# Optimization experiments

Measured on AMD Instinct MI355X. Metric: run time of the kernel, lower is better.

The kernel has to match this reference:

```python
import jax, jax.numpy as jnp
import numpy as np

EMBED = 1024
N_IMG, N_REG = 32, 36
N_CAP, MAX_W = 32, 32
EPS = 1e-8
LAMBDA_SM = 9.0
MARGIN = 0.2
ITER_STEPS = 3


def setup_inputs() -> dict:
    key = jax.random.key(0)
    k = jax.random.split(key, 8)
    img_emb = jax.random.normal(k[0], (N_IMG, N_REG, EMBED), dtype=jnp.float32)
    cap_emb = jax.random.normal(k[1], (N_CAP, MAX_W, EMBED), dtype=jnp.float32)
    cap_lens = jnp.maximum(jax.random.randint(k[2], (N_CAP,), 0, MAX_W + 1), 1)
    s = 1.0 / np.sqrt(2 * EMBED)
    w_lin = jax.random.uniform(k[3], (EMBED, 2 * EMBED), jnp.float32, -s, s)
    b_lin = jax.random.uniform(k[4], (EMBED,), jnp.float32, -s, s)
    w_gate = jax.random.uniform(k[5], (EMBED, 2 * EMBED), jnp.float32, -s, s)
    b_gate = jax.random.uniform(k[6], (EMBED,), jnp.float32, -s, s)
    return {"img_emb": img_emb, "cap_emb": cap_emb, "cap_lens": cap_lens,
            "w_lin": w_lin, "b_lin": b_lin, "w_gate": w_gate, "b_gate": b_gate}


def reference(img_emb, cap_emb, cap_lens, w_lin, b_lin, w_gate, b_gate):
    C, W, D = cap_emb.shape
    I, R, _ = img_emb.shape
    dt = cap_emb.dtype
    # word validity mask replaces the per-caption Python crop to n_word
    mask = (jnp.arange(W)[None, :] < cap_lens[:, None]).astype(dt)  # [C,W]
    cap_e = cap_emb[:, None]                     # [C,1,W,D] fixed query for cosine
    q = jnp.broadcast_to(cap_e, (C, I, W, D))    # evolving query per (cap,img)
    inv_len = 1.0 / cap_lens.astype(dt)          # [C]
    score = jnp.zeros((C, I), dt)
    for _ in range(ITER_STEPS):
        # raw attention: context(images) @ query^T -> [C,I,R,W]
        attn = jnp.einsum('ird,ciwd->cirw', img_emb, q)
        attn = jax.nn.leaky_relu(attn, 0.1)
        # clipped_l2norm over the (valid) word axis
        nrm = jnp.sqrt(jnp.sum(jnp.square(attn * mask[:, None, None, :]),
                               axis=3, keepdims=True)) + EPS
        attn = attn / nrm
        # smooth softmax over regions (per word)
        sm = jax.nn.softmax(attn * LAMBDA_SM, axis=2)
        wc = jnp.einsum('cirw,ird->ciwd', sm, img_emb)  # weighted context [C,I,W,D]
        # cosine similarity between original caption words and attended feats
        w12 = jnp.sum(cap_e * wc, axis=-1)                       # [C,I,W]
        w1 = jnp.sqrt(jnp.sum(jnp.square(cap_e), axis=-1))       # [C,1,W]
        w2 = jnp.sqrt(jnp.sum(jnp.square(wc), axis=-1))          # [C,I,W]
        cos = w12 / jnp.maximum(w1 * w2, EPS)
        score = score + jnp.sum(cos * mask[:, None, :], axis=2) * inv_len[:, None]
        # gated memory fusion (t2i)
        cat = jnp.concatenate([q, wc], axis=-1)                  # [C,I,W,2D]
        h = jnp.tanh(cat @ w_lin.T + b_lin)
        g = jax.nn.sigmoid(cat @ w_gate.T + b_gate)
        q = q * g + h * (1.0 - g)
    # score is [n_caption, n_image] (training-mode transpose in original)
    diag = jnp.diagonal(score)
    cost_s = jnp.clip(MARGIN + score - diag[:, None], 0.0)
    cost_im = jnp.clip(MARGIN + score - diag[None, :], 0.0)
    eye = jnp.eye(C, dtype=bool)
    cost_s = jnp.where(eye, 0.0, cost_s)
    cost_im = jnp.where(eye, 0.0, cost_im)
    return jnp.sum(jnp.max(cost_s, axis=1)) + jnp.sum(jnp.max(cost_im, axis=0))
```

## Files before the change

kernel.cpp:

```cpp
#include <hip/hip_runtime.h>
#include <hip/hip_fp16.h>

#define C_ 32
#define I_ 32
#define W_ 32
#define R_ 36
#define D_ 1024
#define EPS_ 1e-8f
#define LAMBDA_ 9.0f
#define MARGIN_ 0.2f

typedef _Float16 f16;
typedef f16 half8 __attribute__((ext_vector_type(8)));
typedef f16 f16x4 __attribute__((ext_vector_type(4)));
typedef float f32x4 __attribute__((ext_vector_type(4)));

__device__ __forceinline__ void gload16(const void* g, void* l) {
    __builtin_amdgcn_global_load_lds((const __attribute__((address_space(1))) void*)g,
                                     (__attribute__((address_space(3))) void*)l, 16, 0, 0);
}

__device__ __forceinline__ f16x4 to_h4(f32x4 v) {
    f16x4 o; o[0] = (f16)v[0]; o[1] = (f16)v[1]; o[2] = (f16)v[2]; o[3] = (f16)v[3];
    return o;
}

__global__ __launch_bounds__(256) void convert_kernel(
    const float* __restrict__ cap, const float* __restrict__ wl, const float* __restrict__ wg,
    const float* __restrict__ img,
    f16* __restrict__ capH, f16* __restrict__ wlH, f16* __restrict__ wgH, f16* __restrict__ imgH)
{
    const int t = blockIdx.x * 256 + threadIdx.x;
    const float* src; f16* dst; int idx;
    if (t < 262144)        { src = cap; dst = capH; idx = t; }
    else if (t < 786432)   { src = wl;  dst = wlH;  idx = t - 262144; }
    else if (t < 1310720)  { src = wg;  dst = wgH;  idx = t - 786432; }
    else                   { src = img; dst = imgH; idx = t - 1310720; }
    float4 v = ((const float4*)src)[idx];
    f16x4 o; o[0] = (f16)v.x; o[1] = (f16)v.y; o[2] = (f16)v.z; o[3] = (f16)v.w;
    *(f16x4*)(dst + (size_t)idx * 4) = o;
}

__global__ __launch_bounds__(64) void w11_kernel(const float* __restrict__ cap,
                                                 float* __restrict__ w11Buf)
{
    const int row = blockIdx.x;
    const float* p = cap + (size_t)row * 1024;
    float s = 0.f;
    for (int e = threadIdx.x; e < 1024; e += 64) { float v = p[e]; s += v * v; }
    for (int off = 32; off > 0; off >>= 1) s += __shfl_down(s, off);
    if (threadIdx.x == 0) w11Buf[row] = s;
}

__global__ __launch_bounds__(64) void buildmap_kernel(const int* __restrict__ lens,
                                                      int* __restrict__ tileMap,
                                                      int* __restrict__ activeCnt)
{
    if (threadIdx.x == 0) {
        int n = 0;
        for (int cm = 0; cm < 256; cm++) {
            const int len = lens[cm >> 3];
            if ((cm & 7) * 4 < len) tileMap[n++] = cm;
        }
        activeCnt[0] = n;
    }
}

__global__ __launch_bounds__(256) void gram_kernel(const f16* __restrict__ imgH,
                                                   f16* __restrict__ gramH)
{
    __shared__ f16 sG[2][48 * 128];
    const int i = blockIdx.x;
    const int tid = threadIdx.x, lane = tid & 63, wv = tid >> 6;

    auto stage = [&](int b, int k0) {
        for (int g = wv; g < 12; g += 4) {
            const int row = g * 4 + (lane >> 4);
            gload16(imgH + (size_t)(i * 36 + row) * 1024 + k0 + (((lane & 15) ^ (row & 7)) << 3),
                    &sG[b][g * 512]);
        }
    };

    f32x4 acc[4];
    #pragma unroll
    for (int a = 0; a < 4; a++) acc[a] = (f32x4){0.f, 0.f, 0.f, 0.f};

    stage(0, 0);
    __syncthreads();
    int cur = 0;
    for (int kc = 0; kc < 8; kc++) {
        if (kc < 7) stage(cur ^ 1, (kc + 1) * 128);
        #pragma unroll
        for (int ks = 0; ks < 4; ks++) {
            const int arow = wv * 16 + (lane & 15);
            const half8 am = *(const half8*)&sG[cur][arow * 128 + ((((ks << 2) | (lane >> 4)) ^ (arow & 7)) << 3)];
            #pragma unroll
            for (int nt = 0; nt < 4; nt++) {
                const int brow = nt * 16 + (lane & 15);
                const half8 bn = *(const half8*)&sG[cur][brow * 128 + ((((ks << 2) | (lane >> 4)) ^ (brow & 7)) << 3)];
                acc[nt] = __builtin_amdgcn_mfma_f32_16x16x32_f16(am, bn, acc[nt], 0, 0, 0);
            }
        }
        __syncthreads();
        cur ^= 1;
    }
    #pragma unroll
    for (int nt = 0; nt < 4; nt++)
        #pragma unroll
        for (int r = 0; r < 4; r++) {
            const int m = wv * 16 + ((lane >> 4) << 2) + r;
            const int n = nt * 16 + (lane & 15);
            gramH[(size_t)i * 4096 + m * 64 + n] = (m < 36 && n < 36) ? (f16)acc[nt][r] : (f16)0.f;
        }
}

__global__ __launch_bounds__(256) void imgw2t_kernel(
    const f16* __restrict__ wlinH, const f16* __restrict__ wgateH,
    const f16* __restrict__ imgH, f16* __restrict__ imgW2T)
{
    const int jt = blockIdx.x;
    const int i  = blockIdx.y;
    __shared__ f16 sA[128 * 64];
    __shared__ f16 sB[64 * 64];
    const int tid = threadIdx.x, lane = tid & 63, wv = tid >> 6;
    const int wm = wv >> 1, wn = wv & 1;
    f32x4 acc[4][2];
    #pragma unroll
    for (int a = 0; a < 4; a++) { acc[a][0] = (f32x4){0,0,0,0}; acc[a][1] = (f32x4){0,0,0,0}; }

    for (int ks = 0; ks < 16; ks++) {
        const int kk = ks * 64;
        __syncthreads();
        #pragma unroll
        for (int p = 0; p < 4; p++) {
            const int u = tid + p * 256;
            const int row = u >> 3, ch = u & 7;
            const int jr = jt * 128 + row;
            const f16* src = ((jr < 1024) ? (wlinH + (size_t)jr * 2048)
                                          : (wgateH + (size_t)(jr - 1024) * 2048))
                             + 1024 + kk + ((ch ^ (row & 7)) << 3);
            gload16(src, (char*)sA + u * 16);
        }
        #pragma unroll
        for (int p = 0; p < 2; p++) {
            const int u = tid + p * 256;
            const int row = u >> 3, ch = u & 7;
            const f16* src = imgH + (size_t)(i * 36 + row) * 1024 + kk + ((ch ^ (row & 7)) << 3);
            gload16(src, (char*)sB + u * 16);
        }
        __syncthreads();
        #pragma unroll
        for (int ksub = 0; ksub < 2; ksub++) {
            const int kch = (ksub << 2) | (lane >> 4);
            half8 af[4], bf[2];
            #pragma unroll
            for (int tm = 0; tm < 4; tm++) {
                const int row = wm * 64 + tm * 16 + (lane & 15);
                af[tm] = *(const half8*)((const char*)sA + row * 128 + ((kch ^ (row & 7)) << 4));
            }
            #pragma unroll
            for (int tn = 0; tn < 2; tn++) {
                const int row = wn * 32 + tn * 16 + (lane & 15);
                bf[tn] = *(const half8*)((const char*)sB + row * 128 + ((kch ^ (row & 7)) << 4));
            }
            #pragma unroll
            for (int tm = 0; tm < 4; tm++)
                #pragma unroll
                for (int tn = 0; tn < 2; tn++)
                    acc[tm][tn] = __builtin_amdgcn_mfma_f32_16x16x32_f16(af[tm], bf[tn], acc[tm][tn], 0, 0, 0);
        }
    }
    #pragma unroll
    for (int tm = 0; tm < 4; tm++)
        #pragma unroll
        for (int tn = 0; tn < 2; tn++)
            #pragma unroll
            for (int r = 0; r < 4; r++) {
                const int j = jt * 128 + wm * 64 + tm * 16 + (lane >> 4) * 4 + r;
                const int rc = wn * 32 + tn * 16 + (lane & 15);
                imgW2T[((size_t)i * 2048 + j) * 64 + rc] = (rc < 36) ? (f16)acc[tm][tn][r] : (f16)0.f;
            }
}

__device__ __forceinline__ float smt_read(const f16* sSmT, int w, int r) {
    return (float)sSmT[w * 64 + ((((r >> 3) ^ (w & 7)) << 3) | (r & 7))];
}

template<int MODE>
__global__ __launch_bounds__(256, 2) void attn_kernel(
    const f16* __restrict__ imgH,
    const f16* __restrict__ gramH,
    const f16* __restrict__ imgW2T,
    const f16* __restrict__ capH,
    const f16* __restrict__ qcur,
    const f16* __restrict__ capW1,
    f16* __restrict__ capImg0,
    const float* __restrict__ b_lin, const float* __restrict__ b_gate,
    const float* __restrict__ w11Buf,
    const int* __restrict__ lens,
    f16* __restrict__ preLin, f16* __restrict__ preGate,
    f16* __restrict__ qOut,
    float* __restrict__ score)
{
    __shared__ char sBig[57344];
    __shared__ f16 sSmT[2][2048];
    __shared__ float sAttn[36][68];
    __shared__ float sNrm[2][36];
    __shared__ float sW22[2][4][32];
    __shared__ float sW12f[2][32];

    const int bid = blockIdx.x;
    const int cp = bid >> 5;
    const int i  = ((bid & 7) << 2) | ((bid >> 3) & 3);
    const int c0 = cp * 2;
    const int len0 = lens[c0], len1 = lens[c0 + 1];
    const int tid = threadIdx.x;
    const int lane = tid & 63;
    const int wv = tid >> 6;
    const int i36 = i * 36;

    f16 (*sPA)[14336] = (f16(*)[14336])sBig;

    f32x4 accA[3] = {{0,0,0,0},{0,0,0,0},{0,0,0,0}};
    const int lenW = (wv >> 1) ? len1 : len0;
    const bool skipW = (MODE != 0) && ((wv & 1) == 1) && (lenW <= 16);

    auto stageA = [&](int b, int k0) {
        for (int g = wv; g < 28; g += 4) {
            if (g < 12) {
                const int row = g * 4 + (lane >> 4);
                gload16(imgH + (size_t)(i36 + row) * 1024 + k0 + (((lane & 15) ^ (row & 7)) << 3),
                        &sPA[b][g * 512]);
            } else {
                const int gq = g - 12;
                const int w = gq * 4 + (lane >> 4);
                const int lenw = (w >> 5) ? len1 : len0;
                const f16* src = (MODE == 0)
                    ? (capH + (size_t)(c0 * 32 + w) * 1024)
                    : (qcur + (((size_t)(c0 * 32 + w)) * 32 + i) * 1024);
                src += k0 + (((lane & 15) ^ (w & 7)) << 3);
                if (MODE == 0 || (w & 31) < lenw)
                    gload16(src, &sPA[b][6144 + gq * 512]);
            }
        }
    };

    stageA(0, 0);
    __syncthreads();
    int cur = 0;
    for (int kc = 0; kc < 8; kc++) {
        if (kc < 7) stageA(cur ^ 1, (kc + 1) * 128);
        if (!skipW) {
            #pragma unroll
            for (int ks = 0; ks < 4; ks++) {
                const int kch = (ks << 2) | (lane >> 4);
                const int brow = wv * 16 + (lane & 15);
                const half8 bf = *(const half8*)&sPA[cur][6144 + brow * 128 + ((kch ^ (brow & 7)) << 3)];
                #pragma unroll
                for (int mt = 0; mt < 3; mt++) {
                    const int arow = mt * 16 + (lane & 15);
                    const half8 af = *(const half8*)&sPA[cur][arow * 128 + ((kch ^ (arow & 7)) << 3)];
                    accA[mt] = __builtin_amdgcn_mfma_f32_16x16x32_f16(af, bf, accA[mt], 0, 0, 0);
                }
            }
        }
        __syncthreads();
        cur ^= 1;
    }

    if (!skipW) {
        #pragma unroll
        for (int mt = 0; mt < 3; mt++) {
            #pragma unroll
            for (int r = 0; r < 4; r++) {
                const int rr = mt * 16 + (lane >> 4) * 4 + r;
                if (rr < 36) {
                    float v = accA[mt][r];
                    sAttn[rr][wv * 16 + (lane & 15)] = (v >= 0.f) ? v : 0.1f * v;
                }
            }
        }
    }
    __syncthreads();

    if (tid < 72) {
        const int cap = tid / 36;
        const int r = tid - cap * 36;
        const int lenc = cap ? len1 : len0;
        float s = 0.f;
        for (int w = 0; w < lenc; w++) { float v = sAttn[r][cap * 32 + w]; s += v * v; }
        sNrm[cap][r] = LAMBDA_ / (sqrtf(s) + EPS_);
    }
    __syncthreads();

    if (tid < 64) {
        const int cap = tid >> 5, w = tid & 31;
        const int lenc = cap ? len1 : len0;
        f16* smt = &sSmT[cap][0];
        if (w < lenc) {
            float m = -1e30f;
            #pragma unroll
            for (int r = 0; r < 36; r++) m = fmaxf(m, sAttn[r][cap * 32 + w] * sNrm[cap][r]);
            float sum = 0.f;
            #pragma unroll
            for (int r = 0; r < 36; r++) sum += __expf(sAttn[r][cap * 32 + w] * sNrm[cap][r] - m);
            const float inv = 1.0f / sum;
            #pragma unroll
            for (int r = 0; r < 64; r++) {
                const int off = w * 64 + ((((r >> 3) ^ (w & 7)) << 3) | (r & 7));
                smt[off] = (r < 36) ? (f16)(__expf(sAttn[r][cap * 32 + w] * sNrm[cap][r] - m) * inv) : (f16)0.f;
            }
        } else {
            #pragma unroll
            for (int r = 0; r < 64; r++) smt[w * 64 + r] = (f16)0.f;
        }
    }
    __syncthreads();

    if (MODE == 0) {
        const int w = tid >> 3, rg = tid & 7;
        #pragma unroll
        for (int cap = 0; cap < 2; cap++) {
            half8 o;
            #pragma unroll
            for (int k = 0; k < 8; k++) {
                const int r = rg * 8 + k;
                float v = 0.f;
                if (r < 36) { v = sAttn[r][cap * 32 + w]; v = (v >= 0.f) ? v : v * 10.f; }
                o[k] = (f16)v;
            }
            const size_t base = ((((size_t)((c0 + cap) * 32 + i)) << 5) + w) << 6;
            *(half8*)(capImg0 + base + rg * 8) = o;
        }
    }

    half8 af[2][2][2];
    #pragma unroll
    for (int cap = 0; cap < 2; cap++)
        #pragma unroll
        for (int mt = 0; mt < 2; mt++)
            #pragma unroll
            for (int ks = 0; ks < 2; ks++) {
                const int row = mt * 16 + (lane & 15);
                af[cap][mt][ks] = *(const half8*)&sSmT[cap][row * 64 + ((((ks << 2) | (lane >> 4)) ^ (row & 7)) << 3)];
            }

    {
        const f16* gb = gramH + ((size_t)i << 12);
        const int arow = (wv << 4) + (lane & 15);
        const half8 gA0 = *(const half8*)(gb + arow * 64 + ((lane >> 4) << 3));
        const half8 gA1 = *(const half8*)(gb + arow * 64 + 32 + ((lane >> 4) << 3));
        float w22L[2][2] = {{0.f, 0.f}, {0.f, 0.f}};
        #pragma unroll
        for (int cap = 0; cap < 2; cap++)
            #pragma unroll
            for (int mt = 0; mt < 2; mt++) {
                f32x4 t = {0.f, 0.f, 0.f, 0.f};
                t = __builtin_amdgcn_mfma_f32_16x16x32_f16(gA0, af[cap][mt][0], t, 0, 0, 0);
                t = __builtin_amdgcn_mfma_f32_16x16x32_f16(gA1, af[cap][mt][1], t, 0, 0, 0);
                const int w = mt * 16 + (lane & 15);
                const int rp = (wv << 4) + ((lane >> 4) << 2);
                #pragma unroll
                for (int r = 0; r < 4; r++)
                    w22L[cap][mt] += t[r] * smt_read(&sSmT[cap][0], w, rp + r);
            }
        #pragma unroll
        for (int cap = 0; cap < 2; cap++)
            #pragma unroll
            for (int mt = 0; mt < 2; mt++) {
                w22L[cap][mt] += __shfl_xor(w22L[cap][mt], 16);
                w22L[cap][mt] += __shfl_xor(w22L[cap][mt], 32);
            }
        if (lane < 16) {
            #pragma unroll
            for (int cap = 0; cap < 2; cap++) {
                sW22[cap][wv][lane] = w22L[cap][0];
                sW22[cap][wv][16 + lane] = w22L[cap][1];
            }
        }
    }

    {
        const int w = tid >> 3, rg = tid & 7;
        #pragma unroll
        for (int cap = 0; cap < 2; cap++) {
            float p = 0.f;
            if (MODE == 0) {
                #pragma unroll
                for (int k = 0; k < 8; k++) {
                    const int r = rg * 8 + k;
                    if (r < 36) {
                        float v = sAttn[r][cap * 32 + w]; v = (v >= 0.f) ? v : v * 10.f;
                        p += v * smt_read(&sSmT[cap][0], w, r);
                    }
                }
            } else {
                const size_t base = ((((size_t)((c0 + cap) * 32 + i)) << 5) + w) << 6;
                const half8 ci8 = *(const half8*)(capImg0 + base + rg * 8);
                #pragma unroll
                for (int k = 0; k < 8; k++) {
                    const int r = rg * 8 + k;
                    if (r < 36) p += (float)ci8[k] * smt_read(&sSmT[cap][0], w, r);
                }
            }
            p += __shfl_xor(p, 1); p += __shfl_xor(p, 2); p += __shfl_xor(p, 4);
            if (rg == 0) sW12f[cap][w] = p;
        }
    }
    __syncthreads();

    if (tid < 64) {
        const int cap = tid >> 5, w = tid & 31;
        const int lenc = cap ? len1 : len0;
        float part = 0.f;
        if (w < lenc) {
            const float a = sW12f[cap][w];
            const float b = sW22[cap][0][w] + sW22[cap][1][w] + sW22[cap][2][w] + sW22[cap][3][w];
            part = a / fmaxf(sqrtf(w11Buf[(c0 + cap) * 32 + w]) * sqrtf(b), EPS_);
        }
        part += __shfl_down(part, 16);
        part += __shfl_down(part, 8);
        part += __shfl_down(part, 4);
        part += __shfl_down(part, 2);
        part += __shfl_down(part, 1);
        if ((lane & 31) == 0) score[(c0 + cap) * 32 + i] += part / (float)lenc;
    }

    if (MODE == 1) {
        f16 (*tiles)[2][32][66] = (f16(*)[2][32][66])sBig;
        for (int t = 0; t < 32; t++) {
            const int jt_ = t * 4 + wv;
            const int jA = jt_ * 16 + (lane & 15);
            const f16* bb = imgW2T + ((size_t)i * 2048 + jA) * 64;
            const half8 bf0 = *(const half8*)(bb + ((lane >> 4) << 3));
            const half8 bf1 = *(const half8*)(bb + 32 + ((lane >> 4) << 3));
            #pragma unroll
            for (int cap = 0; cap < 2; cap++)
                #pragma unroll
                for (int mt = 0; mt < 2; mt++) {
                    f32x4 acc = {0.f, 0.f, 0.f, 0.f};
                    acc = __builtin_amdgcn_mfma_f32_16x16x32_f16(bf0, af[cap][mt][0], acc, 0, 0, 0);
                    acc = __builtin_amdgcn_mfma_f32_16x16x32_f16(bf1, af[cap][mt][1], acc, 0, 0, 0);
                    const int w = mt * 16 + (lane & 15);
                    *(f16x4*)&tiles[t & 1][cap][w][wv * 16 + ((lane >> 4) << 2)] = to_h4(acc);
                }
            __syncthreads();
            const int w = tid >> 3, jg = tid & 7;
            f16* dst = (t < 16) ? preLin : preGate;
            const int joff = ((t * 64) & 1023) + jg * 8;
            #pragma unroll
            for (int cap = 0; cap < 2; cap++) {
                const int lenc = cap ? len1 : len0;
                if (w < lenc) {
                    const half8 v = *(const half8*)&tiles[t & 1][cap][w][jg * 8];
                    *(half8*)(dst + (((size_t)((c0 + cap) * 32 + w) * 32 + i) << 10) + joff) = v;
                }
            }
        }
    } else if (MODE == 0) {
        f16 (*tiles)[2][2][32][66] = (f16(*)[2][2][32][66])sBig;
        for (int t = 0; t < 16; t++) {
            const int jt_ = t * 4 + wv;
            const int jA = jt_ * 16 + (lane & 15);
            const f16* bbL = imgW2T + ((size_t)i * 2048 + jA) * 64;
            const f16* bbG = imgW2T + ((size_t)i * 2048 + 1024 + jA) * 64;
            const half8 bL0 = *(const half8*)(bbL + ((lane >> 4) << 3));
            const half8 bL1 = *(const half8*)(bbL + 32 + ((lane >> 4) << 3));
            const half8 bG0 = *(const half8*)(bbG + ((lane >> 4) << 3));
            const half8 bG1 = *(const half8*)(bbG + 32 + ((lane >> 4) << 3));
            #pragma unroll
            for (int cap = 0; cap < 2; cap++)
                #pragma unroll
                for (int mt = 0; mt < 2; mt++) {
                    f32x4 aL = {0.f, 0.f, 0.f, 0.f}, aG = {0.f, 0.f, 0.f, 0.f};
                    aL = __builtin_amdgcn_mfma_f32_16x16x32_f16(bL0, af[cap][mt][0], aL, 0, 0, 0);
                    aL = __builtin_amdgcn_mfma_f32_16x16x32_f16(bL1, af[cap][mt][1], aL, 0, 0, 0);
                    aG = __builtin_amdgcn_mfma_f32_16x16x32_f16(bG0, af[cap][mt][0], aG, 0, 0, 0);
                    aG = __builtin_amdgcn_mfma_f32_16x16x32_f16(bG1, af[cap][mt][1], aG, 0, 0, 0);
                    const int w = mt * 16 + (lane & 15);
                    const int x = wv * 16 + ((lane >> 4) << 2);
                    *(f16x4*)&tiles[t & 1][cap][0][w][x] = to_h4(aL);
                    *(f16x4*)&tiles[t & 1][cap][1][w][x] = to_h4(aG);
                }
            __syncthreads();
            const int w = tid >> 3, jg = tid & 7;
            const int j = t * 64 + jg * 8;
            #pragma unroll
            for (int cap = 0; cap < 2; cap++) {
                const int lenc = cap ? len1 : len0;
                if (w < lenc) {
                    const size_t cw = (size_t)((c0 + cap) * 32 + w);
                    const half8 l8 = *(const half8*)&tiles[t & 1][cap][0][w][jg * 8];
                    const half8 g8 = *(const half8*)&tiles[t & 1][cap][1][w][jg * 8];
                    const half8 c1L = *(const half8*)(capW1 + cw * 2048 + j);
                    const half8 c1G = *(const half8*)(capW1 + cw * 2048 + 1024 + j);
                    const half8 cp8 = *(const half8*)(capH + cw * 1024 + j);
                    half8 o;
                    #pragma unroll
                    for (int k = 0; k < 8; k++) {
                        const float h = tanhf((float)l8[k] + (float)c1L[k] + b_lin[j + k]);
                        const float g = 1.f / (1.f + __expf(-((float)g8[k] + (float)c1G[k] + b_gate[j + k])));
                        o[k] = (f16)((float)cp8[k] * g + h * (1.f - g));
                    }
                    *(half8*)(qOut + ((cw * 32 + i) << 10) + j) = o;
                }
            }
        }
    }
}

__global__ __launch_bounds__(256) void qgemm_kernel(
    const f16* __restrict__ Aptr,
    const f16* __restrict__ wlinH, const f16* __restrict__ wgateH,
    const f16* __restrict__ preLin, const f16* __restrict__ preGate,
    const float* __restrict__ b_lin, const float* __restrict__ b_gate,
    f16* __restrict__ outp,
    const int* __restrict__ lens,
    const int* __restrict__ tileMap, const int* __restrict__ activeCnt,
    const int mode)
{
    const int bid = blockIdx.x;
    int jt, cm;
    if (mode) {
        const int x = bid & 7;
        jt = (bid >> 3) & 15;
        const int s = bid >> 7;
        const int a = s * 8 + x;
        if (a >= activeCnt[0]) return;
        cm = tileMap[a];
    } else {
        jt = bid & 15; cm = bid >> 4;
    }
    int len = 32;
    if (mode) len = lens[cm >> 3];
    const int m0 = cm * 128;

    __shared__ f16 sA[128 * 64];
    __shared__ f16 sB[128 * 64];

    const int tid = threadIdx.x;
    const int lane = tid & 63;
    const int wv = tid >> 6;
    const int wm = wv >> 1;
    const int wn = wv & 1;

    f32x4 acc[4][4];
    #pragma unroll
    for (int a = 0; a < 4; a++)
        #pragma unroll
        for (int b = 0; b < 4; b++)
            acc[a][b] = (f32x4){0.f, 0.f, 0.f, 0.f};

    for (int ks = 0; ks < 16; ks++) {
        const int kk = ks * 64;
        #pragma unroll
        for (int p = 0; p < 4; p++) {
            const int idx = tid + p * 256;
            const int row = idx >> 3, ch = idx & 7;
            gload16(Aptr + (size_t)(m0 + row) * 1024 + kk + ((ch ^ (row & 7)) << 3),
                    (char*)sA + idx * 16);
        }
        #pragma unroll
        for (int p = 0; p < 4; p++) {
            const int idx = tid + p * 256;
            const int n = idx >> 3, ch = idx & 7;
            const int j = jt * 64 + (n & 63);
            const f16* wsrc = ((n < 64) ? wlinH : wgateH) + (size_t)j * 2048 + kk + ((ch ^ (n & 7)) << 3);
            gload16(wsrc, (char*)sB + idx * 16);
        }
        __syncthreads();
        #pragma unroll
        for (int ksub = 0; ksub < 2; ksub++) {
            const int k4 = (ksub << 2) | (lane >> 4);
            half8 afr[4], bfr[4];
            #pragma unroll
            for (int tm = 0; tm < 4; tm++) {
                const int row = wm * 64 + tm * 16 + (lane & 15);
                afr[tm] = *(const half8*)((const char*)sA + row * 128 + ((k4 ^ (row & 7)) << 4));
            }
            #pragma unroll
            for (int tn = 0; tn < 4; tn++) {
                const int n = wn * 64 + tn * 16 + (lane & 15);
                bfr[tn] = *(const half8*)((const char*)sB + n * 128 + ((k4 ^ (n & 7)) << 4));
            }
            #pragma unroll
            for (int tm = 0; tm < 4; tm++)
                #pragma unroll
                for (int tn = 0; tn < 4; tn++)
                    acc[tm][tn] = __builtin_amdgcn_mfma_f32_16x16x32_f16(afr[tm], bfr[tn], acc[tm][tn], 0, 0, 0);
        }
        __syncthreads();
    }

    f16 (*tl)[68] = (f16(*)[68])sA;
    f16 (*tg)[68] = (f16(*)[68])sB;
    #pragma unroll
    for (int p = 0; p < 2; p++) {
        __syncthreads();
        if (wm == p) {
            #pragma unroll
            for (int tm = 0; tm < 4; tm++)
                #pragma unroll
                for (int tn = 0; tn < 4; tn++) {
                    const int n = wn * 64 + tn * 16 + (lane & 15);
                    #pragma unroll
                    for (int r = 0; r < 4; r++) {
                        const int ml = tm * 16 + ((lane >> 4) << 2) + r;
                        if (n < 64) tl[ml][n] = (f16)acc[tm][tn][r];
                        else        tg[ml][n - 64] = (f16)acc[tm][tn][r];
                    }
                }
        }
        __syncthreads();
        const int rl = tid >> 2;
        const int gm = m0 + p * 64 + rl;
        const int j0 = (tid & 3) * 16;
        const int j = jt * 64 + j0;
        bool active = true;
        if (mode) active = (((gm >> 5) & 31) < len);
        if (active) {
            const half8 l0 = *(const half8*)&tl[rl][j0];
            const half8 l1 = *(const half8*)&tl[rl][j0 + 8];
            const half8 g0 = *(const half8*)&tg[rl][j0];
            const half8 g1 = *(const half8*)&tg[rl][j0 + 8];
            if (mode == 0) {
                *(half8*)(outp + (size_t)gm * 2048 + j) = l0;
                *(half8*)(outp + (size_t)gm * 2048 + j + 8) = l1;
                *(half8*)(outp + (size_t)gm * 2048 + 1024 + j) = g0;
                *(half8*)(outp + (size_t)gm * 2048 + 1024 + j + 8) = g1;
            } else {
                const size_t off = ((size_t)gm << 10) + j;
                const half8 pl0 = *(const half8*)(preLin + off);
                const half8 pl1 = *(const half8*)(preLin + off + 8);
                const half8 pg0 = *(const half8*)(preGate + off);
                const half8 pg1 = *(const half8*)(preGate + off + 8);
                const half8 qo0 = *(const half8*)(Aptr + off);
                const half8 qo1 = *(const half8*)(Aptr + off + 8);
                half8 o0, o1;
                #pragma unroll
                for (int k = 0; k < 8; k++) {
                    const float h = tanhf((float)l0[k] + (float)pl0[k] + b_lin[j + k]);
                    const float g = 1.f / (1.f + __expf(-((float)g0[k] + (float)pg0[k] + b_gate[j + k])));
                    o0[k] = (f16)((float)qo0[k] * g + h * (1.f - g));
                }
                #pragma unroll
                for (int k = 0; k < 8; k++) {
                    const float h = tanhf((float)l1[k] + (float)pl1[k] + b_lin[j + 8 + k]);
                    const float g = 1.f / (1.f + __expf(-((float)g1[k] + (float)pg1[k] + b_gate[j + 8 + k])));
                    o1[k] = (f16)((float)qo1[k] * g + h * (1.f - g));
                }
                *(half8*)(outp + off) = o0;
                *(half8*)(outp + off + 8) = o1;
            }
        }
    }
}

__global__ __launch_bounds__(64) void loss_kernel(const float* __restrict__ score,
                                                  float* __restrict__ out)
{
    __shared__ float s[32][33];
    __shared__ float diag[32];
    const int tid = threadIdx.x;
    for (int idx = tid; idx < 1024; idx += 64) s[idx >> 5][idx & 31] = score[idx];
    __syncthreads();
    if (tid < 32) diag[tid] = s[tid][tid];
    __syncthreads();
    float total = 0.f;
    if (tid < 32) {
        float m1 = 0.f, m2 = 0.f;
        for (int k = 0; k < 32; k++) {
            if (k != tid) {
                m1 = fmaxf(m1, fmaxf(0.f, MARGIN_ + s[tid][k] - diag[tid]));
                m2 = fmaxf(m2, fmaxf(0.f, MARGIN_ + s[k][tid] - diag[tid]));
            }
        }
        total = m1 + m2;
    }
    for (int off = 32; off > 0; off >>= 1) total += __shfl_down(total, off);
    if (tid == 0) out[0] = total;
}

extern "C" void kernel_launch(void* const* d_in, const int* in_sizes, int n_in,
                              void* d_out, int out_size, void* d_ws, size_t ws_size,
                              hipStream_t stream) {
    const float* img    = (const float*)d_in[0];
    const float* cap    = (const float*)d_in[1];
    const int*   lens   = (const int*)d_in[2];
    const float* w_lin  = (const float*)d_in[3];
    const float* b_lin  = (const float*)d_in[4];
    const float* w_gate = (const float*)d_in[5];
    const float* b_gate = (const float*)d_in[6];
    float* out = (float*)d_out;

    char* ws = (char*)d_ws;
    f16* qA      = (f16*)(ws);
    f16* preLin  = (f16*)(ws + 67108864);
    f16* preGate = (f16*)(ws + 134217728);
    f16* capH    = (f16*)(ws + 201326592);
    f16* wlinH   = (f16*)(ws + 203423744);
    f16* wgateH  = (f16*)(ws + 207618048);
    f16* imgH    = (f16*)(ws + 211812352);
    f16* gramH   = (f16*)(ws + 214958080);
    f16* capImg0 = (f16*)(ws + 216006656);
    f16* imgW2T  = (f16*)(ws + 220200960);
    f16* capW1   = (f16*)(ws + 228589568);
    float* w11Buf = (float*)(ws + 232783872);
    float* score  = (float*)(ws + 232787968);
    int* tileMap  = (int*)(ws + 232792064);
    int* activeCnt= (int*)(ws + 232793088);
    f16* qB = preLin;

    hipMemsetAsync(score, 0, C_ * I_ * sizeof(float), stream);
    convert_kernel<<<dim3(6272), dim3(256), 0, stream>>>(cap, w_lin, w_gate, img, capH, wlinH, wgateH, imgH);
    w11_kernel<<<dim3(1024), dim3(64), 0, stream>>>(cap, w11Buf);
    buildmap_kernel<<<dim3(1), dim3(64), 0, stream>>>(lens, tileMap, activeCnt);
    gram_kernel<<<dim3(32), dim3(256), 0, stream>>>(imgH, gramH);
    imgw2t_kernel<<<dim3(16, 32), dim3(256), 0, stream>>>(wlinH, wgateH, imgH, imgW2T);
    qgemm_kernel<<<dim3(128), dim3(256), 0, stream>>>(capH, wlinH, wgateH, (const f16*)0, (const f16*)0,
                                                      b_lin, b_gate, capW1, lens, tileMap, activeCnt, 0);
    attn_kernel<0><<<dim3(512), dim3(256), 0, stream>>>(imgH, gramH, imgW2T, capH, (const f16*)0,
                                                        capW1, capImg0, b_lin, b_gate, w11Buf, lens,
                                                        preLin, preGate, qA, score);
    attn_kernel<1><<<dim3(512), dim3(256), 0, stream>>>(imgH, gramH, imgW2T, capH, qA,
                                                        capW1, capImg0, b_lin, b_gate, w11Buf, lens,
                                                        preLin, preGate, (f16*)0, score);
    qgemm_kernel<<<dim3(2432), dim3(256), 0, stream>>>(qA, wlinH, wgateH, preLin, preGate,
                                                       b_lin, b_gate, qB, lens, tileMap, activeCnt, 1);
    attn_kernel<2><<<dim3(512), dim3(256), 0, stream>>>(imgH, gramH, imgW2T, capH, qB,
                                                        capW1, capImg0, b_lin, b_gate, w11Buf, lens,
                                                        preLin, preGate, (f16*)0, score);

    loss_kernel<<<dim3(1), dim3(64), 0, stream>>>(score, out);
}
```

Baseline: 422.4 us.

## Single-buffer attn staging to raise occupancy, fold buildmap into w11, hoist biases

The attn kernel's double-buffered shared staging is replaced with a single buffer sized per mode, and the launch bound rises from 2 to 3 blocks per CU. The aim is more resident blocks, at the cost of exposing global-to-LDS load latency because loads no longer overlap the MFMA compute and each k-step now needs an extra barrier. The buildmap launch is merged into w11_kernel to save a kernel launch. Bias loads in the qgemm epilogue are hoisted into vector registers.

```diff
diff --git a/kernel.cpp b/kernel.cpp
--- a/kernel.cpp
+++ b/kernel.cpp
@@ -42,28 +42,25 @@
 }
 
 __global__ __launch_bounds__(64) void w11_kernel(const float* __restrict__ cap,
-                                                 float* __restrict__ w11Buf)
+                                                 float* __restrict__ w11Buf,
+                                                 const int* __restrict__ lens,
+                                                 int* __restrict__ tileMap,
+                                                 int* __restrict__ activeCnt)
 {
+    if (blockIdx.x == 0 && threadIdx.x == 63) {
+        int n = 0;
+        for (int cm = 0; cm < 256; cm++) {
+            const int len = lens[cm >> 3];
+            if ((cm & 7) * 4 < len) tileMap[n++] = cm;
+        }
+        activeCnt[0] = n;
+    }
     const int row = blockIdx.x;
     const float* p = cap + (size_t)row * 1024;
     float s = 0.f;
     for (int e = threadIdx.x; e < 1024; e += 64) { float v = p[e]; s += v * v; }
     for (int off = 32; off > 0; off >>= 1) s += __shfl_down(s, off);
     if (threadIdx.x == 0) w11Buf[row] = s;
-}
-
-__global__ __launch_bounds__(64) void buildmap_kernel(const int* __restrict__ lens,
-                                                      int* __restrict__ tileMap,
-                                                      int* __restrict__ activeCnt)
-{
-    if (threadIdx.x == 0) {
-        int n = 0;
-        for (int cm = 0; cm < 256; cm++) {
-            const int len = lens[cm >> 3];
-            if ((cm & 7) * 4 < len) tileMap[n++] = cm;
-        }
-        activeCnt[0] = n;
-    }
 }
 
 __global__ __launch_bounds__(256) void gram_kernel(const f16* __restrict__ imgH,
@@ -187,7 +184,7 @@
 }
 
 template<int MODE>
-__global__ __launch_bounds__(256, 2) void attn_kernel(
+__global__ __launch_bounds__(256, 3) void attn_kernel(
     const f16* __restrict__ imgH,
     const f16* __restrict__ gramH,
     const f16* __restrict__ imgW2T,
@@ -202,9 +199,10 @@
     f16* __restrict__ qOut,
     float* __restrict__ score)
 {
-    __shared__ char sBig[57344];
+    constexpr int SBIG = (MODE == 0) ? 33792 : 28672;
+    __shared__ __align__(16) char sBig[SBIG];
     __shared__ f16 sSmT[2][2048];
-    __shared__ float sAttn[36][68];
+    __shared__ float sAttn[36][66];
     __shared__ float sNrm[2][36];
     __shared__ float sW22[2][4][32];
     __shared__ float sW12f[2][32];
@@ -219,18 +217,18 @@
     const int wv = tid >> 6;
     const int i36 = i * 36;
 
-    f16 (*sPA)[14336] = (f16(*)[14336])sBig;
+    f16* sPA = (f16*)sBig;
 
     f32x4 accA[3] = {{0,0,0,0},{0,0,0,0},{0,0,0,0}};
     const int lenW = (wv >> 1) ? len1 : len0;
     const bool skipW = (MODE != 0) && ((wv & 1) == 1) && (lenW <= 16);
 
-    auto stageA = [&](int b, int k0) {
+    auto stageA = [&](int k0) {
         for (int g = wv; g < 28; g += 4) {
             if (g < 12) {
                 const int row = g * 4 + (lane >> 4);
                 gload16(imgH + (size_t)(i36 + row) * 1024 + k0 + (((lane & 15) ^ (row & 7)) << 3),
-                        &sPA[b][g * 512]);
+                        &sPA[g * 512]);
             } else {
                 const int gq = g - 12;
                 const int w = gq * 4 + (lane >> 4);
@@ -240,32 +238,29 @@
                     : (qcur + (((size_t)(c0 * 32 + w)) * 32 + i) * 1024);
                 src += k0 + (((lane & 15) ^ (w & 7)) << 3);
                 if (MODE == 0 || (w & 31) < lenw)
-                    gload16(src, &sPA[b][6144 + gq * 512]);
+                    gload16(src, &sPA[6144 + gq * 512]);
             }
         }
     };
 
-    stageA(0, 0);
-    __syncthreads();
-    int cur = 0;
     for (int kc = 0; kc < 8; kc++) {
-        if (kc < 7) stageA(cur ^ 1, (kc + 1) * 128);
+        stageA(kc * 128);
+        __syncthreads();
         if (!skipW) {
             #pragma unroll
             for (int ks = 0; ks < 4; ks++) {
                 const int kch = (ks << 2) | (lane >> 4);
                 const int brow = wv * 16 + (lane & 15);
-                const half8 bf = *(const half8*)&sPA[cur][6144 + brow * 128 + ((kch ^ (brow & 7)) << 3)];
+                const half8 bf = *(const half8*)&sPA[6144 + brow * 128 + ((kch ^ (brow & 7)) << 3)];
                 #pragma unroll
                 for (int mt = 0; mt < 3; mt++) {
                     const int arow = mt * 16 + (lane & 15);
-                    const half8 af = *(const half8*)&sPA[cur][arow * 128 + ((kch ^ (arow & 7)) << 3)];
+                    const half8 af = *(const half8*)&sPA[arow * 128 + ((kch ^ (arow & 7)) << 3)];
                     accA[mt] = __builtin_amdgcn_mfma_f32_16x16x32_f16(af, bf, accA[mt], 0, 0, 0);
                 }
             }
         }
         __syncthreads();
-        cur ^= 1;
     }
 
     if (!skipW) {
@@ -594,6 +589,16 @@
 
     f16 (*tl)[68] = (f16(*)[68])sA;
     f16 (*tg)[68] = (f16(*)[68])sB;
+    const int j0 = (tid & 3) * 16;
+    const int j = jt * 64 + j0;
+    f32x4 blv[4], bgv[4];
+    if (mode == 1) {
+        #pragma unroll
+        for (int q = 0; q < 4; q++) {
+            blv[q] = *(const f32x4*)(b_lin + j + q * 4);
+            bgv[q] = *(const f32x4*)(b_gate + j + q * 4);
+        }
+    }
     #pragma unroll
     for (int p = 0; p < 2; p++) {
         __syncthreads();
@@ -614,8 +619,6 @@
         __syncthreads();
         const int rl = tid >> 2;
         const int gm = m0 + p * 64 + rl;
-        const int j0 = (tid & 3) * 16;
-        const int j = jt * 64 + j0;
         bool active = true;
         if (mode) active = (((gm >> 5) & 31) < len);
         if (active) {
@@ -639,14 +642,14 @@
                 half8 o0, o1;
                 #pragma unroll
                 for (int k = 0; k < 8; k++) {
-                    const float h = tanhf((float)l0[k] + (float)pl0[k] + b_lin[j + k]);
-                    const float g = 1.f / (1.f + __expf(-((float)g0[k] + (float)pg0[k] + b_gate[j + k])));
+                    const float h = tanhf((float)l0[k] + (float)pl0[k] + blv[k >> 2][k & 3]);
+                    const float g = 1.f / (1.f + __expf(-((float)g0[k] + (float)pg0[k] + bgv[k >> 2][k & 3])));
                     o0[k] = (f16)((float)qo0[k] * g + h * (1.f - g));
                 }
                 #pragma unroll
                 for (int k = 0; k < 8; k++) {
-                    const float h = tanhf((float)l1[k] + (float)pl1[k] + b_lin[j + 8 + k]);
-                    const float g = 1.f / (1.f + __expf(-((float)g1[k] + (float)pg1[k] + b_gate[j + 8 + k])));
+                    const float h = tanhf((float)l1[k] + (float)pl1[k] + blv[2 + (k >> 2)][k & 3]);
+                    const float g = 1.f / (1.f + __expf(-((float)g1[k] + (float)pg1[k] + bgv[2 + (k >> 2)][k & 3])));
                     o1[k] = (f16)((float)qo1[k] * g + h * (1.f - g));
                 }
                 *(half8*)(outp + off) = o0;
@@ -713,8 +716,7 @@
 
     hipMemsetAsync(score, 0, C_ * I_ * sizeof(float), stream);
     convert_kernel<<<dim3(6272), dim3(256), 0, stream>>>(cap, w_lin, w_gate, img, capH, wlinH, wgateH, imgH);
-    w11_kernel<<<dim3(1024), dim3(64), 0, stream>>>(cap, w11Buf);
-    buildmap_kernel<<<dim3(1), dim3(64), 0, stream>>>(lens, tileMap, activeCnt);
+    w11_kernel<<<dim3(1024), dim3(64), 0, stream>>>(cap, w11Buf, lens, tileMap, activeCnt);
     gram_kernel<<<dim3(32), dim3(256), 0, stream>>>(imgH, gramH);
     imgw2t_kernel<<<dim3(16, 32), dim3(256), 0, stream>>>(wlinH, wgateH, imgH, imgW2T);
     qgemm_kernel<<<dim3(128), dim3(256), 0, stream>>>(capH, wlinH, wgateH, (const f16*)0, (const f16*)0,
```

Result: faster. 411.7 us (-2.5%).
